# Kernel tuning notes

Hardware: AMD Instinct MI355X
Metric: run time of the kernel (lower is better)

## Reference

```python
import jax, jax.numpy as jnp
import numpy as np

B, C_IN, H, W = 64, 2048, 14, 14
D, FF, G, NC, NH = 768, 2048, 100, 9605, 8
DF = int(NC / G + 0.999)  # 97
HD = D // NH
EPS = 1e-5


def _ln(x, g, b):
    m = jnp.mean(x, axis=-1, keepdims=True)
    v = jnp.mean(jnp.square(x - m), axis=-1, keepdims=True)
    return (x - m) * jax.lax.rsqrt(v + EPS) * g + b


def setup_inputs() -> dict:
    key = jax.random.key(0)
    ks = jax.random.split(key, 16)
    def xav(k, shape):
        fan_in, fan_out = shape[-1], shape[-2] if len(shape) > 1 else shape[-1]
        std = float(np.sqrt(2.0 / (fan_in + fan_out)))
        return jax.random.normal(k, shape, jnp.float32) * std
    return {
        "x": jax.random.normal(ks[0], (B, C_IN, H, W), jnp.float32),
        "w_embed": xav(ks[1], (D, C_IN)), "b_embed": jnp.zeros((D,), jnp.float32),
        "query_embed": jax.random.normal(ks[2], (G, D), jnp.float32),
        "wq": xav(ks[3], (D, D)), "bq": jnp.zeros((D,), jnp.float32),
        "wk": xav(ks[4], (D, D)), "bk": jnp.zeros((D,), jnp.float32),
        "wv": xav(ks[5], (D, D)), "bv": jnp.zeros((D,), jnp.float32),
        "wo": xav(ks[6], (D, D)), "bo": jnp.zeros((D,), jnp.float32),
        "g1": jnp.ones((D,), jnp.float32), "be1": jnp.zeros((D,), jnp.float32),
        "g2": jnp.ones((D,), jnp.float32), "be2": jnp.zeros((D,), jnp.float32),
        "g3": jnp.ones((D,), jnp.float32), "be3": jnp.zeros((D,), jnp.float32),
        "w1": xav(ks[7], (FF, D)), "bl1": jnp.zeros((FF,), jnp.float32),
        "w2": xav(ks[8], (D, FF)), "bl2": jnp.zeros((D,), jnp.float32),
        "dup_pool": xav(ks[9], (G, D, DF)),
        "dup_bias": jnp.zeros((NC,), jnp.float32),
    }


def reference(x, w_embed, b_embed, query_embed, wq, bq, wk, bk, wv, bv, wo, bo,
              g1, be1, g2, be2, g3, be3, w1, bl1, w2, bl2, dup_pool, dup_bias):
    bs = x.shape[0]
    # [B, C, H, W] -> [B, S, C]
    mem = x.reshape(bs, x.shape[1], -1).transpose(0, 2, 1)
    # embed_standart + relu -> [B, S, D]
    mem = jax.nn.relu(jnp.einsum('bsc,dc->bsd', mem, w_embed) + b_embed)
    # tgt = queries broadcast to batch: [B, G, D]
    tgt = jnp.broadcast_to(query_embed[None], (bs, G, D))
    # layer: tgt = norm1(tgt + dropout1(tgt)) = norm1(2*tgt)
    tgt = _ln(tgt + tgt, g1, be1)
    # cross multihead attention (q=tgt, k=v=mem)
    q = (jnp.einsum('bgd,ed->bge', tgt, wq) + bq).reshape(bs, G, NH, HD)
    k = (jnp.einsum('bsd,ed->bse', mem, wk) + bk).reshape(bs, -1, NH, HD)
    v = (jnp.einsum('bsd,ed->bse', mem, wv) + bv).reshape(bs, -1, NH, HD)
    scores = jnp.einsum('bghd,bshd->bhgs', q, k) / jnp.sqrt(jnp.float32(HD))
    attn = jax.nn.softmax(scores, axis=-1)
    ctx = jnp.einsum('bhgs,bshd->bghd', attn, v).reshape(bs, G, D)
    ctx = jnp.einsum('bgd,ed->bge', ctx, wo) + bo
    tgt = _ln(tgt + ctx, g2, be2)
    # FFN
    ff = jax.nn.relu(jnp.einsum('bgd,fd->bgf', tgt, w1) + bl1)
    ff = jnp.einsum('bgf,df->bgd', ff, w2) + bl2
    h = _ln(tgt + ff, g3, be3)  # [B, G, D]
    # grouped FC: per-group matmul fused into one batched einsum
    out_extrap = jnp.einsum('bgd,gdf->bgf', h, dup_pool)  # [B, G, DF]
    logits = out_extrap.reshape(bs, G * DF)[:, :NC] + dup_bias
    return logits
```

## Files before the change

kernel.cpp:

```cpp
#include <hip/hip_runtime.h>
#include <hip/hip_bf16.h>


#define B_    64
#define CIN_  2048
#define S_    196
#define D_    768
#define FF_   2048
#define G_    100
#define NC_   9605
#define NH_   8
#define HD_   96
#define DF_   97
#define FP_   112
#define GP_   112
#define SP_   224
#define BS_   (B_ * S_)
#define BG_   (B_ * G_)

typedef __bf16 bf16x8 __attribute__((ext_vector_type(8)));
typedef float  f32x4  __attribute__((ext_vector_type(4)));

__device__ __forceinline__ float bf2f(ushort u) {
  union { unsigned int i; float f; } v; v.i = ((unsigned int)u) << 16; return v.f;
}
__device__ __forceinline__ ushort f2bf(float f) {
  __hip_bfloat16 h = __float2bfloat16(f);
  return *reinterpret_cast<ushort*>(&h);
}

__device__ __forceinline__ void gl2lds16(const ushort* g, ushort* l) {
  __builtin_amdgcn_global_load_lds((const __attribute__((address_space(1))) unsigned int*)g,
                                   (__attribute__((address_space(3))) unsigned int*)l, 16, 0, 0);
}

struct CvtArgs {
  const float* src[7];
  ushort*      dst[7];
  int          n4[7];
  int          total;
};
__global__ void k_cvtall(CvtArgs a) {
  int i = blockIdx.x * blockDim.x + threadIdx.x;
  const int stride = gridDim.x * blockDim.x;
  for (; i < a.total; i += stride) {
    int seg = 0, off = i;
    while (off >= a.n4[seg]) { off -= a.n4[seg]; ++seg; }
    float4 v = ((const float4*)a.src[seg])[off];
    ushort4 o;
    o.x = f2bf(v.x); o.y = f2bf(v.y); o.z = f2bf(v.z); o.w = f2bf(v.w);
    ((ushort4*)a.dst[seg])[off] = o;
  }
}

__global__ __launch_bounds__(256) void k_xpose(const float* __restrict__ x, ushort* __restrict__ A) {
  __shared__ float tile[32][33];
  const int c0 = blockIdx.x * 32, s0 = blockIdx.y * 32, b = blockIdx.z;
  const int t = threadIdx.x;
  const int tx = t & 31, ty = t >> 5;
  const float* xb = x + (size_t)b * CIN_ * S_;
  #pragma unroll
  for (int r = 0; r < 32; r += 8) {
    int c = c0 + ty + r, s = s0 + tx;
    tile[ty + r][tx] = (s < S_) ? xb[(size_t)c * S_ + s] : 0.f;
  }
  __syncthreads();
  const int sl = t >> 3, cq = (t & 7) * 4;
  const int s = s0 + sl;
  if (s < S_) {
    ushort4 o;
    o.x = f2bf(tile[cq + 0][sl]);
    o.y = f2bf(tile[cq + 1][sl]);
    o.z = f2bf(tile[cq + 2][sl]);
    o.w = f2bf(tile[cq + 3][sl]);
    *(ushort4*)&A[((size_t)(b * S_ + s)) * CIN_ + c0 + cq] = o;
  }
}

__global__ __launch_bounds__(256) void k_dupT(const float* __restrict__ dup, ushort* __restrict__ dupT) {
  __shared__ float tile[32][33];
  const int f0 = blockIdx.x * 32, d0 = blockIdx.y * 32, g = blockIdx.z;
  const int tx = threadIdx.x & 31, ty = threadIdx.x >> 5;
  #pragma unroll
  for (int r = 0; r < 32; r += 8) {
    int d = d0 + ty + r, f = f0 + tx;
    tile[ty + r][tx] = (f < DF_) ? dup[(size_t)g * D_ * DF_ + (size_t)d * DF_ + f] : 0.f;
  }
  __syncthreads();
  #pragma unroll
  for (int r = 0; r < 32; r += 8) {
    int f = f0 + ty + r, d = d0 + tx;
    if (f < FP_) dupT[((size_t)g * FP_ + f) * D_ + d] = f2bf(tile[tx][ty + r]);
  }
}

__global__ __launch_bounds__(256) void k_tgt(const float* __restrict__ qe,
    const float* __restrict__ g1, const float* __restrict__ be1,
    float* __restrict__ tgt, ushort* __restrict__ tgtB) {
  const int g = blockIdx.x, t = threadIdx.x;
  if (g >= G_) {
    for (int d = t; d < D_; d += 256) tgtB[(size_t)g * D_ + d] = 0;
    return;
  }
  __shared__ float r1[256], r2[256];
  float y[3]; float s = 0.f, sq = 0.f;
  const float* row = qe + (size_t)g * D_;
  #pragma unroll
  for (int i = 0; i < 3; ++i) { float v = 2.f * row[t + i * 256]; y[i] = v; s += v; sq += v * v; }
  r1[t] = s; r2[t] = sq; __syncthreads();
  for (int o = 128; o > 0; o >>= 1) { if (t < o) { r1[t] += r1[t + o]; r2[t] += r2[t + o]; } __syncthreads(); }
  const float mean = r1[0] * (1.f / D_);
  const float var  = r2[0] * (1.f / D_) - mean * mean;
  const float w = rsqrtf(var + 1e-5f);
  #pragma unroll
  for (int i = 0; i < 3; ++i) {
    int d = t + i * 256;
    float v = (y[i] - mean) * w * g1[d] + be1[d];
    tgt[(size_t)g * D_ + d] = v;
    tgtB[(size_t)g * D_ + d] = f2bf(v);
  }
}

__global__ __launch_bounds__(256) void k_gemm(const ushort* __restrict__ A, const ushort* __restrict__ B,
    const float* __restrict__ bias, const float* __restrict__ bias2,
    float* __restrict__ Cf, ushort* __restrict__ Cb, ushort* __restrict__ Vt,
    int N, int K, int nbx, int nm, int relu) {
  const int l = blockIdx.x;
  const int mb = (l >> 3) / nbx * 8 + (l & 7);
  const int nb = (l >> 3) % nbx;
  if (mb >= nm) return;
  __shared__ ushort As[128 * 32];
  __shared__ ushort Bs[128 * 32];
  const int t = threadIdx.x;
  const int m0 = mb * 128, n0 = nb * 128;
  const int lane = t & 63, wave = t >> 6;
  const int quad = lane >> 4, lrow = lane & 15;
  const int wr = (wave >> 1) * 64, wc = (wave & 1) * 64;
  const int srow = t >> 2, scol = (t & 3) * 8;
  f32x4 acc[4][4] = {};
  for (int k0 = 0; k0 < K; k0 += 32) {
    const ushort* ag = A + (size_t)(m0 + srow) * K + k0 + scol;
    const ushort* bg = B + (size_t)(n0 + srow) * K + k0 + scol;
    gl2lds16(ag,                    &As[srow * 32 + scol]);
    gl2lds16(ag + (size_t)64 * K,   &As[(srow + 64) * 32 + scol]);
    gl2lds16(bg,                    &Bs[srow * 32 + scol]);
    gl2lds16(bg + (size_t)64 * K,   &Bs[(srow + 64) * 32 + scol]);
    __syncthreads();
    bf16x8 af[4], bfr[4];
    #pragma unroll
    for (int i = 0; i < 4; ++i) af[i] = *(const bf16x8*)&As[(wr + i * 16 + lrow) * 32 + quad * 8];
    #pragma unroll
    for (int j = 0; j < 4; ++j) bfr[j] = *(const bf16x8*)&Bs[(wc + j * 16 + lrow) * 32 + quad * 8];
    #pragma unroll
    for (int i = 0; i < 4; ++i)
      #pragma unroll
      for (int j = 0; j < 4; ++j)
        acc[i][j] = __builtin_amdgcn_mfma_f32_16x16x32_bf16(af[i], bfr[j], acc[i][j], 0, 0, 0);
    __syncthreads();
  }
  #pragma unroll
  for (int i = 0; i < 4; ++i) {
    #pragma unroll
    for (int j = 0; j < 4; ++j) {
      const int gcol = n0 + wc + j * 16 + lrow;
      const float bv = (bias2 && gcol >= D_) ? bias2[gcol - D_] : (bias ? bias[gcol] : 0.f);
      if (Vt && gcol >= D_) {
        const int dv = gcol - D_, hh = dv / HD_, hd = dv % HD_;
        const int row0 = m0 + wr + i * 16 + quad * 4;
        const int bb = row0 / S_, ss = row0 % S_;
        ushort4 o;
        o.x = f2bf(acc[i][j][0] + bv);
        o.y = f2bf(acc[i][j][1] + bv);
        o.z = f2bf(acc[i][j][2] + bv);
        o.w = f2bf(acc[i][j][3] + bv);
        *(ushort4*)&Vt[((size_t)(bb * NH_ + hh) * HD_ + hd) * SP_ + ss] = o;
      } else {
        #pragma unroll
        for (int r = 0; r < 4; ++r) {
          const int grow = m0 + wr + i * 16 + quad * 4 + r;
          float v = acc[i][j][r] + bv;
          if (relu) v = fmaxf(v, 0.f);
          if (Cf) Cf[(size_t)grow * N + gcol] = v;
          else    Cb[(size_t)grow * N + gcol] = f2bf(v);
        }
      }
    }
  }
}
static inline int swz_grid(int nm, int nbx) { return ((nm + 7) & ~7) * nbx; }

__global__ __launch_bounds__(256) void k_attn(const ushort* __restrict__ qB,
    const ushort* __restrict__ Kb, const ushort* __restrict__ VbT, ushort* __restrict__ ctx) {
  __shared__ ushort lds[GP_ * SP_];
  ushort* Ks = lds;
  ushort* Ps = lds;
  const int h = blockIdx.x, b = blockIdx.y, t = threadIdx.x;
  const int bh = b * NH_ + h;
  const int lane = t & 63, wave = t >> 6;
  const int quad = lane >> 4, c = lane & 15;
  for (int i = t; i < 208 * 12; i += 256) {
    int r = i / 12, col = (i % 12) * 8;
    gl2lds16(Kb + ((size_t)(b * S_ + r)) * D_ + h * HD_ + col, &Ks[i * 8]);
  }
  __syncthreads();
  const float scale = 0.1020620726f;
  f32x4 p[2][13];
  #pragma unroll
  for (int rep = 0; rep < 2; ++rep) {
    const int ii = wave + rep * 4;
    if (ii >= 7) continue;
    bf16x8 af[3];
    #pragma unroll
    for (int ks = 0; ks < 3; ++ks)
      af[ks] = *(const bf16x8*)(qB + ((size_t)(ii * 16 + c)) * D_ + h * HD_ + ks * 32 + quad * 8);
    #pragma unroll
    for (int j = 0; j < 13; ++j) {
      f32x4 a = {};
      #pragma unroll
      for (int ks = 0; ks < 3; ++ks) {
        bf16x8 bf = *(const bf16x8*)&Ks[(j * 16 + c) * HD_ + ks * 32 + quad * 8];
        a = __builtin_amdgcn_mfma_f32_16x16x32_bf16(af[ks], bf, a, 0, 0, 0);
      }
      p[rep][j] = a;
    }
    float m[4] = {-1e30f, -1e30f, -1e30f, -1e30f};
    #pragma unroll
    for (int j = 0; j < 13; ++j)
      #pragma unroll
      for (int r = 0; r < 4; ++r) {
        float v = p[rep][j][r] * scale;
        if (j == 12 && c >= 4) v = -1e30f;
        p[rep][j][r] = v;
        m[r] = fmaxf(m[r], v);
      }
    #pragma unroll
    for (int r = 0; r < 4; ++r) {
      m[r] = fmaxf(m[r], __shfl_xor(m[r], 1));
      m[r] = fmaxf(m[r], __shfl_xor(m[r], 2));
      m[r] = fmaxf(m[r], __shfl_xor(m[r], 4));
      m[r] = fmaxf(m[r], __shfl_xor(m[r], 8));
    }
    float lsum[4] = {0.f, 0.f, 0.f, 0.f};
    #pragma unroll
    for (int j = 0; j < 13; ++j)
      #pragma unroll
      for (int r = 0; r < 4; ++r) {
        float e = __expf(p[rep][j][r] - m[r]);
        p[rep][j][r] = e; lsum[r] += e;
      }
    #pragma unroll
    for (int r = 0; r < 4; ++r) {
      lsum[r] += __shfl_xor(lsum[r], 1);
      lsum[r] += __shfl_xor(lsum[r], 2);
      lsum[r] += __shfl_xor(lsum[r], 4);
      lsum[r] += __shfl_xor(lsum[r], 8);
      lsum[r] = 1.f / lsum[r];
    }
    #pragma unroll
    for (int j = 0; j < 13; ++j)
      #pragma unroll
      for (int r = 0; r < 4; ++r)
        p[rep][j][r] *= lsum[r];
  }
  __syncthreads();
  #pragma unroll
  for (int rep = 0; rep < 2; ++rep) {
    const int ii = wave + rep * 4;
    if (ii >= 7) continue;
    #pragma unroll
    for (int r = 0; r < 4; ++r) {
      const int g = ii * 16 + quad * 4 + r;
      #pragma unroll
      for (int j = 0; j < 13; ++j)
        Ps[g * SP_ + j * 16 + c] = f2bf(p[rep][j][r]);
      Ps[g * SP_ + 208 + c] = 0;
    }
  }
  __syncthreads();
  #pragma unroll
  for (int rep = 0; rep < 2; ++rep) {
    const int ii = wave + rep * 4;
    if (ii >= 7) continue;
    bf16x8 af[7];
    #pragma unroll
    for (int k = 0; k < 7; ++k)
      af[k] = *(const bf16x8*)&Ps[(ii * 16 + c) * SP_ + k * 32 + quad * 8];
    #pragma unroll
    for (int j = 0; j < 6; ++j) {
      f32x4 acc = {};
      #pragma unroll
      for (int k = 0; k < 7; ++k) {
        bf16x8 bf = *(const bf16x8*)(VbT + ((size_t)bh * HD_ + j * 16 + c) * SP_ + k * 32 + quad * 8);
        acc = __builtin_amdgcn_mfma_f32_16x16x32_bf16(af[k], bf, acc, 0, 0, 0);
      }
      #pragma unroll
      for (int r = 0; r < 4; ++r) {
        const int g = ii * 16 + quad * 4 + r;
        if (g < G_)
          ctx[((size_t)(b * G_ + g)) * D_ + h * HD_ + j * 16 + c] = f2bf(acc[r]);
      }
    }
  }
}

__global__ __launch_bounds__(256) void k_lnres(const float* __restrict__ resid, int resid_mod,
    const float* __restrict__ add, const float* __restrict__ gamma, const float* __restrict__ beta,
    float* __restrict__ outf, ushort* __restrict__ outb, int transb) {
  const int row = blockIdx.x, t = threadIdx.x;
  __shared__ float r1[256], r2[256];
  const float* rrow = resid + (size_t)(resid_mod ? (row % G_) : row) * D_;
  const float* arow = add + (size_t)row * D_;
  float y[3]; float s = 0.f, sq = 0.f;
  #pragma unroll
  for (int i = 0; i < 3; ++i) {
    int d = t + i * 256;
    float v = rrow[d] + arow[d];
    y[i] = v; s += v; sq += v * v;
  }
  r1[t] = s; r2[t] = sq; __syncthreads();
  for (int o = 128; o > 0; o >>= 1) { if (t < o) { r1[t] += r1[t + o]; r2[t] += r2[t + o]; } __syncthreads(); }
  const float mean = r1[0] * (1.f / D_);
  const float var  = r2[0] * (1.f / D_) - mean * mean;
  const float w = rsqrtf(var + 1e-5f);
  const size_t orow = transb ? ((size_t)(row % G_) * B_ + row / G_) : (size_t)row;
  #pragma unroll
  for (int i = 0; i < 3; ++i) {
    int d = t + i * 256;
    float v = (y[i] - mean) * w * gamma[d] + beta[d];
    if (outf) outf[(size_t)row * D_ + d] = v;
    if (outb) outb[orow * D_ + d] = f2bf(v);
  }
}

__global__ __launch_bounds__(256) void k_head4(const ushort* __restrict__ hT,
    const ushort* __restrict__ dupT, const float* __restrict__ dup_bias, float* __restrict__ out) {
  const int g = blockIdx.x, j = blockIdx.y, t = threadIdx.x;
  const int lane = t & 63, wave = t >> 6;
  const int quad = lane >> 4, c = lane & 15;
  const ushort* ap = hT + ((size_t)g * B_ + wave * 16 + c) * D_;
  const ushort* bp = dupT + ((size_t)g * FP_ + j * 16 + c) * D_;
  f32x4 acc = {};
  #pragma unroll 8
  for (int k0 = 0; k0 < D_; k0 += 32) {
    bf16x8 af = *(const bf16x8*)(ap + k0 + quad * 8);
    bf16x8 bf = *(const bf16x8*)(bp + k0 + quad * 8);
    acc = __builtin_amdgcn_mfma_f32_16x16x32_bf16(af, bf, acc, 0, 0, 0);
  }
  const int f = j * 16 + c;
  if (f >= DF_) return;
  const int n = g * DF_ + f;
  if (n >= NC_) return;
  const float bv = dup_bias[n];
  #pragma unroll
  for (int r = 0; r < 4; ++r) {
    const int b = wave * 16 + quad * 4 + r;
    out[(size_t)b * NC_ + n] = acc[r] + bv;
  }
}

static constexpr size_t OFF_AEMB  = 0;
static constexpr size_t OFF_VBT   = 0;
static constexpr size_t OFF_FF    = 0;
static constexpr size_t OFF_FFO   = 26214400;
static constexpr size_t OFF_WEMB  = 51380224;
static constexpr size_t OFF_MEM   = 54525952;
static constexpr size_t OFF_WK    = 73793536;
static constexpr size_t OFF_WV    = 74973184;
static constexpr size_t OFF_WO    = 76152832;
static constexpr size_t OFF_W1    = 77332480;
static constexpr size_t OFF_W2    = 80478208;
static constexpr size_t OFF_DUP   = 83623936;
static constexpr size_t OFF_KB    = 100827136;
static constexpr size_t OFF_TGT   = 139362304;
static constexpr size_t OFF_TGTB  = 139669504;
static constexpr size_t OFF_Q     = 139866112;
static constexpr size_t OFF_CTX   = 140068864;
static constexpr size_t OFF_WQ    = OFF_CTX;
static constexpr size_t OFF_CTXO  = 149899264;
static constexpr size_t OFF_TGT2F = 169560064;
static constexpr size_t OFF_TGT2B = 189220864;
static constexpr size_t OFF_HB    = 199051264;

extern "C" void kernel_launch(void* const* d_in, const int* in_sizes, int n_in,
                              void* d_out, int out_size, void* d_ws, size_t ws_size,
                              hipStream_t stream) {
  const float* x           = (const float*)d_in[0];
  const float* w_embed     = (const float*)d_in[1];
  const float* b_embed     = (const float*)d_in[2];
  const float* query_embed = (const float*)d_in[3];
  const float* wq          = (const float*)d_in[4];
  const float* bq          = (const float*)d_in[5];
  const float* wk          = (const float*)d_in[6];
  const float* bk          = (const float*)d_in[7];
  const float* wv          = (const float*)d_in[8];
  const float* bv          = (const float*)d_in[9];
  const float* wo          = (const float*)d_in[10];
  const float* bo          = (const float*)d_in[11];
  const float* g1          = (const float*)d_in[12];
  const float* be1         = (const float*)d_in[13];
  const float* g2          = (const float*)d_in[14];
  const float* be2         = (const float*)d_in[15];
  const float* g3          = (const float*)d_in[16];
  const float* be3         = (const float*)d_in[17];
  const float* w1          = (const float*)d_in[18];
  const float* bl1         = (const float*)d_in[19];
  const float* w2          = (const float*)d_in[20];
  const float* bl2         = (const float*)d_in[21];
  const float* dup_pool    = (const float*)d_in[22];
  const float* dup_bias    = (const float*)d_in[23];
  float* out = (float*)d_out;
  char* ws = (char*)d_ws;

  ushort* aemb  = (ushort*)(ws + OFF_AEMB);
  ushort* wembB = (ushort*)(ws + OFF_WEMB);
  ushort* memB  = (ushort*)(ws + OFF_MEM);
  ushort* wkvB  = (ushort*)(ws + OFF_WK);
  ushort* wkB   = (ushort*)(ws + OFF_WK);
  ushort* wvB   = (ushort*)(ws + OFF_WV);
  ushort* woB   = (ushort*)(ws + OFF_WO);
  ushort* w1B   = (ushort*)(ws + OFF_W1);
  ushort* w2B   = (ushort*)(ws + OFF_W2);
  ushort* wqB   = (ushort*)(ws + OFF_WQ);
  ushort* dupT  = (ushort*)(ws + OFF_DUP);
  ushort* Kb    = (ushort*)(ws + OFF_KB);
  float*  tgtF  = (float*)(ws + OFF_TGT);
  ushort* tgtB  = (ushort*)(ws + OFF_TGTB);
  ushort* qB    = (ushort*)(ws + OFF_Q);
  ushort* VbT   = (ushort*)(ws + OFF_VBT);
  ushort* ctxB  = (ushort*)(ws + OFF_CTX);
  float*  ctxoF = (float*)(ws + OFF_CTXO);
  float*  tgt2F = (float*)(ws + OFF_TGT2F);
  ushort* tgt2B = (ushort*)(ws + OFF_TGT2B);
  ushort* ffB   = (ushort*)(ws + OFF_FF);
  float*  ffoF  = (float*)(ws + OFF_FFO);
  ushort* hT    = (ushort*)(ws + OFF_HB);

  CvtArgs ca;
  ca.src[0] = w_embed; ca.dst[0] = wembB; ca.n4[0] = D_ * CIN_ / 4;
  ca.src[1] = wk;      ca.dst[1] = wkB;   ca.n4[1] = D_ * D_ / 4;
  ca.src[2] = wv;      ca.dst[2] = wvB;   ca.n4[2] = D_ * D_ / 4;
  ca.src[3] = wo;      ca.dst[3] = woB;   ca.n4[3] = D_ * D_ / 4;
  ca.src[4] = w1;      ca.dst[4] = w1B;   ca.n4[4] = FF_ * D_ / 4;
  ca.src[5] = w2;      ca.dst[5] = w2B;   ca.n4[5] = D_ * FF_ / 4;
  ca.src[6] = wq;      ca.dst[6] = wqB;   ca.n4[6] = D_ * D_ / 4;
  ca.total = ca.n4[0] + ca.n4[1] + ca.n4[2] + ca.n4[3] + ca.n4[4] + ca.n4[5] + ca.n4[6];
  k_cvtall<<<2048, 256, 0, stream>>>(ca);
  k_dupT<<<dim3(4, 24, G_), 256, 0, stream>>>(dup_pool, dupT);

  k_xpose<<<dim3(CIN_ / 32, 7, B_), 256, 0, stream>>>(x, aemb);

  k_tgt<<<128, 256, 0, stream>>>(query_embed, g1, be1, tgtF, tgtB);

  k_gemm<<<swz_grid(1, 6), 256, 0, stream>>>(tgtB, wqB, bq, nullptr, nullptr, qB, nullptr,
                                             D_, D_, 6, 1, 0);

  k_gemm<<<swz_grid(98, 6), 256, 0, stream>>>(aemb, wembB, b_embed, nullptr, nullptr, memB, nullptr,
                                              D_, CIN_, 6, 98, 1);

  k_gemm<<<swz_grid(98, 12), 256, 0, stream>>>(memB, wkvB, bk, bv, nullptr, Kb, VbT,
                                               D_, D_, 12, 98, 0);

  k_attn<<<dim3(NH_, B_), 256, 0, stream>>>(qB, Kb, VbT, ctxB);

  k_gemm<<<swz_grid(50, 6), 256, 0, stream>>>(ctxB, woB, bo, nullptr, ctxoF, nullptr, nullptr,
                                              D_, D_, 6, 50, 0);

  k_lnres<<<BG_, 256, 0, stream>>>(tgtF, 1, ctxoF, g2, be2, tgt2F, tgt2B, 0);

  k_gemm<<<swz_grid(50, 16), 256, 0, stream>>>(tgt2B, w1B, bl1, nullptr, nullptr, ffB, nullptr,
                                               FF_, D_, 16, 50, 1);
  k_gemm<<<swz_grid(50, 6), 256, 0, stream>>>(ffB, w2B, bl2, nullptr, ffoF, nullptr, nullptr,
                                              D_, FF_, 6, 50, 0);

  k_lnres<<<BG_, 256, 0, stream>>>(tgt2F, 0, ffoF, g3, be3, nullptr, hT, 1);

  k_head4<<<dim3(G_, 7), 256, 0, stream>>>(hT, dupT, dup_bias, out);
}
```

Measured before the change: 612.3 us.

## Merge prep kernels into one launch, fold Q projection into embed GEMM, bf16 intermediates

Folds the transpose, dup-pool transpose, weight conversion and query layernorm kernels into a single heterogeneous prep kernel that dispatches on block index. The small Q-projection GEMM now runs as extra blocks appended to the embed GEMM grid. The out-projection and FFN2 outputs are stored as bf16 instead of fp32 before the residual layernorms. Together these cut launch count and intermediate memory traffic, at the cost of coarser prep blocks that loop over more tiles and lower precision in the residual adds.

Measured after the change: 581.7 us. 5.0% less time.

```diff
diff --git a/kernel.cpp b/kernel.cpp
--- a/kernel.cpp
+++ b/kernel.cpp
@@ -34,77 +34,98 @@
                                    (__attribute__((address_space(3))) unsigned int*)l, 16, 0, 0);
 }
 
-struct CvtArgs {
-  const float* src[7];
-  ushort*      dst[7];
-  int          n4[7];
-  int          total;
+#define XP_BLKS 1792
+#define DT_BLKS 400
+#define CV_BLKS 512
+#define TG_BLKS 128
+
+struct PrepArgs {
+  const float* x;   ushort* aemb;
+  const float* dup; ushort* dupT;
+  const float* csrc[7]; ushort* cdst[7]; int cn4[7]; int ctotal;
+  const float* qe; const float* g1; const float* be1;
+  float* tgt; ushort* tgtB;
 };
-__global__ void k_cvtall(CvtArgs a) {
-  int i = blockIdx.x * blockDim.x + threadIdx.x;
-  const int stride = gridDim.x * blockDim.x;
-  for (; i < a.total; i += stride) {
-    int seg = 0, off = i;
-    while (off >= a.n4[seg]) { off -= a.n4[seg]; ++seg; }
-    float4 v = ((const float4*)a.src[seg])[off];
-    ushort4 o;
-    o.x = f2bf(v.x); o.y = f2bf(v.y); o.z = f2bf(v.z); o.w = f2bf(v.w);
-    ((ushort4*)a.dst[seg])[off] = o;
-  }
-}
-
-__global__ __launch_bounds__(256) void k_xpose(const float* __restrict__ x, ushort* __restrict__ A) {
+
+__global__ __launch_bounds__(256) void k_prep(PrepArgs pa) {
   __shared__ float tile[32][33];
-  const int c0 = blockIdx.x * 32, s0 = blockIdx.y * 32, b = blockIdx.z;
+  __shared__ float r1[256], r2[256];
+  int jid = blockIdx.x;
   const int t = threadIdx.x;
-  const int tx = t & 31, ty = t >> 5;
-  const float* xb = x + (size_t)b * CIN_ * S_;
-  #pragma unroll
-  for (int r = 0; r < 32; r += 8) {
-    int c = c0 + ty + r, s = s0 + tx;
-    tile[ty + r][tx] = (s < S_) ? xb[(size_t)c * S_ + s] : 0.f;
-  }
-  __syncthreads();
-  const int sl = t >> 3, cq = (t & 7) * 4;
-  const int s = s0 + sl;
-  if (s < S_) {
-    ushort4 o;
-    o.x = f2bf(tile[cq + 0][sl]);
-    o.y = f2bf(tile[cq + 1][sl]);
-    o.z = f2bf(tile[cq + 2][sl]);
-    o.w = f2bf(tile[cq + 3][sl]);
-    *(ushort4*)&A[((size_t)(b * S_ + s)) * CIN_ + c0 + cq] = o;
-  }
-}
-
-__global__ __launch_bounds__(256) void k_dupT(const float* __restrict__ dup, ushort* __restrict__ dupT) {
-  __shared__ float tile[32][33];
-  const int f0 = blockIdx.x * 32, d0 = blockIdx.y * 32, g = blockIdx.z;
-  const int tx = threadIdx.x & 31, ty = threadIdx.x >> 5;
-  #pragma unroll
-  for (int r = 0; r < 32; r += 8) {
-    int d = d0 + ty + r, f = f0 + tx;
-    tile[ty + r][tx] = (f < DF_) ? dup[(size_t)g * D_ * DF_ + (size_t)d * DF_ + f] : 0.f;
-  }
-  __syncthreads();
-  #pragma unroll
-  for (int r = 0; r < 32; r += 8) {
-    int f = f0 + ty + r, d = d0 + tx;
-    if (f < FP_) dupT[((size_t)g * FP_ + f) * D_ + d] = f2bf(tile[tx][ty + r]);
-  }
-}
-
-__global__ __launch_bounds__(256) void k_tgt(const float* __restrict__ qe,
-    const float* __restrict__ g1, const float* __restrict__ be1,
-    float* __restrict__ tgt, ushort* __restrict__ tgtB) {
-  const int g = blockIdx.x, t = threadIdx.x;
+
+  if (jid < XP_BLKS) {
+    const int b = jid / 28, rem = jid % 28;
+    const int s0 = (rem % 7) * 32, cbase = (rem / 7) * 512;
+    const int tx = t & 31, ty = t >> 5;
+    const int sl = t >> 3, cq = (t & 7) * 4;
+    const float* xb = pa.x + (size_t)b * CIN_ * S_;
+    for (int cc = 0; cc < 512; cc += 32) {
+      const int c0 = cbase + cc;
+      #pragma unroll
+      for (int r = 0; r < 32; r += 8) {
+        int c = c0 + ty + r, s = s0 + tx;
+        tile[ty + r][tx] = (s < S_) ? xb[(size_t)c * S_ + s] : 0.f;
+      }
+      __syncthreads();
+      const int s = s0 + sl;
+      if (s < S_) {
+        ushort4 o;
+        o.x = f2bf(tile[cq + 0][sl]); o.y = f2bf(tile[cq + 1][sl]);
+        o.z = f2bf(tile[cq + 2][sl]); o.w = f2bf(tile[cq + 3][sl]);
+        *(ushort4*)&pa.aemb[((size_t)(b * S_ + s)) * CIN_ + c0 + cq] = o;
+      }
+      __syncthreads();
+    }
+    return;
+  }
+  jid -= XP_BLKS;
+
+  if (jid < DT_BLKS) {
+    const int g = jid >> 2, dchunk = jid & 3;
+    const int tx = t & 31, ty = t >> 5;
+    for (int di = 0; di < 6; ++di) {
+      const int d0 = dchunk * 192 + di * 32;
+      for (int f0 = 0; f0 < 128; f0 += 32) {
+        #pragma unroll
+        for (int r = 0; r < 32; r += 8) {
+          int d = d0 + ty + r, f = f0 + tx;
+          tile[ty + r][tx] = (f < DF_) ? pa.dup[(size_t)g * D_ * DF_ + (size_t)d * DF_ + f] : 0.f;
+        }
+        __syncthreads();
+        #pragma unroll
+        for (int r = 0; r < 32; r += 8) {
+          int f = f0 + ty + r, d = d0 + tx;
+          if (f < FP_) pa.dupT[((size_t)g * FP_ + f) * D_ + d] = f2bf(tile[tx][ty + r]);
+        }
+        __syncthreads();
+      }
+    }
+    return;
+  }
+  jid -= DT_BLKS;
+
+  if (jid < CV_BLKS) {
+    int i = jid * 256 + t;
+    const int stride = CV_BLKS * 256;
+    for (; i < pa.ctotal; i += stride) {
+      int seg = 0, off = i;
+      while (off >= pa.cn4[seg]) { off -= pa.cn4[seg]; ++seg; }
+      float4 v = ((const float4*)pa.csrc[seg])[off];
+      ushort4 o;
+      o.x = f2bf(v.x); o.y = f2bf(v.y); o.z = f2bf(v.z); o.w = f2bf(v.w);
+      ((ushort4*)pa.cdst[seg])[off] = o;
+    }
+    return;
+  }
+  jid -= CV_BLKS;
+
+  const int g = jid;
   if (g >= G_) {
-    for (int d = t; d < D_; d += 256) tgtB[(size_t)g * D_ + d] = 0;
+    for (int d = t; d < D_; d += 256) pa.tgtB[(size_t)g * D_ + d] = 0;
     return;
   }
-  __shared__ float r1[256], r2[256];
   float y[3]; float s = 0.f, sq = 0.f;
-  const float* row = qe + (size_t)g * D_;
+  const float* row = pa.qe + (size_t)g * D_;
   #pragma unroll
   for (int i = 0; i < 3; ++i) { float v = 2.f * row[t + i * 256]; y[i] = v; s += v; sq += v * v; }
   r1[t] = s; r2[t] = sq; __syncthreads();
@@ -115,24 +136,17 @@
   #pragma unroll
   for (int i = 0; i < 3; ++i) {
     int d = t + i * 256;
-    float v = (y[i] - mean) * w * g1[d] + be1[d];
-    tgt[(size_t)g * D_ + d] = v;
-    tgtB[(size_t)g * D_ + d] = f2bf(v);
-  }
-}
-
-__global__ __launch_bounds__(256) void k_gemm(const ushort* __restrict__ A, const ushort* __restrict__ B,
+    float v = (y[i] - mean) * w * pa.g1[d] + pa.be1[d];
+    pa.tgt[(size_t)g * D_ + d] = v;
+    pa.tgtB[(size_t)g * D_ + d] = f2bf(v);
+  }
+}
+
+__device__ __forceinline__ void gemm_core(const ushort* __restrict__ A, const ushort* __restrict__ B,
     const float* __restrict__ bias, const float* __restrict__ bias2,
     float* __restrict__ Cf, ushort* __restrict__ Cb, ushort* __restrict__ Vt,
-    int N, int K, int nbx, int nm, int relu) {
-  const int l = blockIdx.x;
-  const int mb = (l >> 3) / nbx * 8 + (l & 7);
-  const int nb = (l >> 3) % nbx;
-  if (mb >= nm) return;
-  __shared__ ushort As[128 * 32];
-  __shared__ ushort Bs[128 * 32];
+    int N, int K, int m0, int n0, int relu, ushort* As, ushort* Bs) {
   const int t = threadIdx.x;
-  const int m0 = mb * 128, n0 = nb * 128;
   const int lane = t & 63, wave = t >> 6;
   const int quad = lane >> 4, lrow = lane & 15;
   const int wr = (wave >> 1) * 64, wc = (wave & 1) * 64;
@@ -187,6 +201,26 @@
     }
   }
 }
+
+__global__ __launch_bounds__(256) void k_gemm(const ushort* __restrict__ A, const ushort* __restrict__ B,
+    const float* __restrict__ bias, const float* __restrict__ bias2,
+    float* __restrict__ Cf, ushort* __restrict__ Cb, ushort* __restrict__ Vt,
+    int N, int K, int nbx, int nm, int relu,
+    const ushort* __restrict__ A2, const ushort* __restrict__ B2,
+    const float* __restrict__ bias_2, ushort* __restrict__ Cb2, int N2, int K2) {
+  __shared__ ushort As[128 * 32];
+  __shared__ ushort Bs[128 * 32];
+  const int l = blockIdx.x;
+  const int base = ((nm + 7) & ~7) * nbx;
+  if (l >= base) {
+    gemm_core(A2, B2, bias_2, nullptr, nullptr, Cb2, nullptr, N2, K2, 0, (l - base) * 128, 0, As, Bs);
+    return;
+  }
+  const int mb = (l >> 3) / nbx * 8 + (l & 7);
+  const int nb = (l >> 3) % nbx;
+  if (mb >= nm) return;
+  gemm_core(A, B, bias, bias2, Cf, Cb, Vt, N, K, mb * 128, nb * 128, relu, As, Bs);
+}
 static inline int swz_grid(int nm, int nbx) { return ((nm + 7) & ~7) * nbx; }
 
 __global__ __launch_bounds__(256) void k_attn(const ushort* __restrict__ qB,
@@ -304,17 +338,17 @@
 }
 
 __global__ __launch_bounds__(256) void k_lnres(const float* __restrict__ resid, int resid_mod,
-    const float* __restrict__ add, const float* __restrict__ gamma, const float* __restrict__ beta,
+    const ushort* __restrict__ addB, const float* __restrict__ gamma, const float* __restrict__ beta,
     float* __restrict__ outf, ushort* __restrict__ outb, int transb) {
   const int row = blockIdx.x, t = threadIdx.x;
   __shared__ float r1[256], r2[256];
   const float* rrow = resid + (size_t)(resid_mod ? (row % G_) : row) * D_;
-  const float* arow = add + (size_t)row * D_;
+  const ushort* arow = addB + (size_t)row * D_;
   float y[3]; float s = 0.f, sq = 0.f;
   #pragma unroll
   for (int i = 0; i < 3; ++i) {
     int d = t + i * 256;
-    float v = rrow[d] + arow[d];
+    float v = rrow[d] + bf2f(arow[d]);
     y[i] = v; s += v; sq += v * v;
   }
   r1[t] = s; r2[t] = sq; __syncthreads();
@@ -428,51 +462,51 @@
   ushort* qB    = (ushort*)(ws + OFF_Q);
   ushort* VbT   = (ushort*)(ws + OFF_VBT);
   ushort* ctxB  = (ushort*)(ws + OFF_CTX);
-  float*  ctxoF = (float*)(ws + OFF_CTXO);
+  ushort* ctxoB = (ushort*)(ws + OFF_CTXO);
   float*  tgt2F = (float*)(ws + OFF_TGT2F);
   ushort* tgt2B = (ushort*)(ws + OFF_TGT2B);
   ushort* ffB   = (ushort*)(ws + OFF_FF);
-  float*  ffoF  = (float*)(ws + OFF_FFO);
+  ushort* ffoB  = (ushort*)(ws + OFF_FFO);
   ushort* hT    = (ushort*)(ws + OFF_HB);
 
-  CvtArgs ca;
-  ca.src[0] = w_embed; ca.dst[0] = wembB; ca.n4[0] = D_ * CIN_ / 4;
-  ca.src[1] = wk;      ca.dst[1] = wkB;   ca.n4[1] = D_ * D_ / 4;
-  ca.src[2] = wv;      ca.dst[2] = wvB;   ca.n4[2] = D_ * D_ / 4;
-  ca.src[3] = wo;      ca.dst[3] = woB;   ca.n4[3] = D_ * D_ / 4;
-  ca.src[4] = w1;      ca.dst[4] = w1B;   ca.n4[4] = FF_ * D_ / 4;
-  ca.src[5] = w2;      ca.dst[5] = w2B;   ca.n4[5] = D_ * FF_ / 4;
-  ca.src[6] = wq;      ca.dst[6] = wqB;   ca.n4[6] = D_ * D_ / 4;
-  ca.total = ca.n4[0] + ca.n4[1] + ca.n4[2] + ca.n4[3] + ca.n4[4] + ca.n4[5] + ca.n4[6];
-  k_cvtall<<<2048, 256, 0, stream>>>(ca);
-  k_dupT<<<dim3(4, 24, G_), 256, 0, stream>>>(dup_pool, dupT);
-
-  k_xpose<<<dim3(CIN_ / 32, 7, B_), 256, 0, stream>>>(x, aemb);
-
-  k_tgt<<<128, 256, 0, stream>>>(query_embed, g1, be1, tgtF, tgtB);
-
-  k_gemm<<<swz_grid(1, 6), 256, 0, stream>>>(tgtB, wqB, bq, nullptr, nullptr, qB, nullptr,
-                                             D_, D_, 6, 1, 0);
-
-  k_gemm<<<swz_grid(98, 6), 256, 0, stream>>>(aemb, wembB, b_embed, nullptr, nullptr, memB, nullptr,
-                                              D_, CIN_, 6, 98, 1);
+  PrepArgs pa;
+  pa.x = x; pa.aemb = aemb;
+  pa.dup = dup_pool; pa.dupT = dupT;
+  pa.csrc[0] = w_embed; pa.cdst[0] = wembB; pa.cn4[0] = D_ * CIN_ / 4;
+  pa.csrc[1] = wk;      pa.cdst[1] = wkB;   pa.cn4[1] = D_ * D_ / 4;
+  pa.csrc[2] = wv;      pa.cdst[2] = wvB;   pa.cn4[2] = D_ * D_ / 4;
+  pa.csrc[3] = wo;      pa.cdst[3] = woB;   pa.cn4[3] = D_ * D_ / 4;
+  pa.csrc[4] = w1;      pa.cdst[4] = w1B;   pa.cn4[4] = FF_ * D_ / 4;
+  pa.csrc[5] = w2;      pa.cdst[5] = w2B;   pa.cn4[5] = D_ * FF_ / 4;
+  pa.csrc[6] = wq;      pa.cdst[6] = wqB;   pa.cn4[6] = D_ * D_ / 4;
+  pa.ctotal = pa.cn4[0] + pa.cn4[1] + pa.cn4[2] + pa.cn4[3] + pa.cn4[4] + pa.cn4[5] + pa.cn4[6];
+  pa.qe = query_embed; pa.g1 = g1; pa.be1 = be1; pa.tgt = tgtF; pa.tgtB = tgtB;
+  k_prep<<<XP_BLKS + DT_BLKS + CV_BLKS + TG_BLKS, 256, 0, stream>>>(pa);
+
+  k_gemm<<<swz_grid(98, 6) + 6, 256, 0, stream>>>(aemb, wembB, b_embed, nullptr,
+                                                  nullptr, memB, nullptr, D_, CIN_, 6, 98, 1,
+                                                  tgtB, wqB, bq, qB, D_, D_);
 
   k_gemm<<<swz_grid(98, 12), 256, 0, stream>>>(memB, wkvB, bk, bv, nullptr, Kb, VbT,
-                                               D_, D_, 12, 98, 0);
+                                               D_, D_, 12, 98, 0,
+                                               nullptr, nullptr, nullptr, nullptr, 0, 0);
 
   k_attn<<<dim3(NH_, B_), 256, 0, stream>>>(qB, Kb, VbT, ctxB);
 
-  k_gemm<<<swz_grid(50, 6), 256, 0, stream>>>(ctxB, woB, bo, nullptr, ctxoF, nullptr, nullptr,
-                                              D_, D_, 6, 50, 0);
-
-  k_lnres<<<BG_, 256, 0, stream>>>(tgtF, 1, ctxoF, g2, be2, tgt2F, tgt2B, 0);
+  k_gemm<<<swz_grid(50, 6), 256, 0, stream>>>(ctxB, woB, bo, nullptr, nullptr, ctxoB, nullptr,
+                                              D_, D_, 6, 50, 0,
+                                              nullptr, nullptr, nullptr, nullptr, 0, 0);
+
+  k_lnres<<<BG_, 256, 0, stream>>>(tgtF, 1, ctxoB, g2, be2, tgt2F, tgt2B, 0);
 
   k_gemm<<<swz_grid(50, 16), 256, 0, stream>>>(tgt2B, w1B, bl1, nullptr, nullptr, ffB, nullptr,
-                                               FF_, D_, 16, 50, 1);
-  k_gemm<<<swz_grid(50, 6), 256, 0, stream>>>(ffB, w2B, bl2, nullptr, ffoF, nullptr, nullptr,
-                                              D_, FF_, 6, 50, 0);
-
-  k_lnres<<<BG_, 256, 0, stream>>>(tgt2F, 0, ffoF, g3, be3, nullptr, hT, 1);
+                                               FF_, D_, 16, 50, 1,
+                                               nullptr, nullptr, nullptr, nullptr, 0, 0);
+  k_gemm<<<swz_grid(50, 6), 256, 0, stream>>>(ffB, w2B, bl2, nullptr, nullptr, ffoB, nullptr,
+                                              D_, FF_, 6, 50, 0,
+                                              nullptr, nullptr, nullptr, nullptr, 0, 0);
+
+  k_lnres<<<BG_, 256, 0, stream>>>(tgt2F, 0, ffoB, g3, be3, nullptr, hT, 1);
 
   k_head4<<<dim3(G_, 7), 256, 0, stream>>>(hT, dupT, dup_bias, out);
 }
```
